# Kernel tuning notes

Hardware: AMD Instinct MI355X
Metric: run time of the kernel (lower is better)

Reference implementation:

```python
import jax, jax.numpy as jnp
import numpy as np

H, MEL, ATT, TXT = 1024, 80, 640, 640   # n_hidden, n_mel, n_attn_channels, n_text+n_speaker
T, TTXT = 600, 128


def setup_inputs() -> dict:
    key = jax.random.key(0)
    ks = jax.random.split(key, 20)
    def w(k, shape, s=0.02):
        return (jax.random.normal(k, shape) * s).astype(jnp.float32)
    return {
        "residual": jax.random.normal(ks[0], (T, 1, MEL), jnp.float32),
        "text": jax.random.normal(ks[1], (TTXT, 1, TXT), jnp.float32),
        # attention_lstm: LSTM(MEL -> H), 1 layer
        "Wih_a": w(ks[2], (4 * H, MEL)), "Whh_a": w(ks[3], (4 * H, H)),
        "bih_a": jnp.zeros(4 * H, jnp.float32), "bhh_a": jnp.zeros(4 * H, jnp.float32),
        # Attention: query/key/value projections + scoring vector v
        "Wq": w(ks[4], (ATT, H)), "Wk": w(ks[5], (ATT, TXT)), "Wv": w(ks[6], (ATT, TXT)),
        "v_w": w(ks[7], (ATT,)),
        # decoder lstm: LSTM(H+ATT -> H), 2 layers
        "Wih0": w(ks[8], (4 * H, H + ATT)), "Whh0": w(ks[9], (4 * H, H)),
        "bih0": jnp.zeros(4 * H, jnp.float32), "bhh0": jnp.zeros(4 * H, jnp.float32),
        "Wih1": w(ks[10], (4 * H, H)), "Whh1": w(ks[11], (4 * H, H)),
        "bih1": jnp.zeros(4 * H, jnp.float32), "bhh1": jnp.zeros(4 * H, jnp.float32),
        # DenseLayer: two tanh(Linear(H,H))
        "D0w": w(ks[12], (H, H)), "D0b": jnp.zeros(H, jnp.float32),
        "D1w": w(ks[13], (H, H)), "D1b": jnp.zeros(H, jnp.float32),
        # Conv1d(H, 2*MEL, kernel=1) == Linear
        "conv_w": w(ks[14], (2 * MEL, H)), "conv_b": jnp.zeros(2 * MEL, jnp.float32),
        # gate layer: Linear(H+ATT, 1)
        "gate_w": w(ks[15], (H + ATT,)), "gate_b": jnp.zeros((), jnp.float32),
    }


def lstm_cell(x, h, c, Wih, Whh, bih, bhh):
    # PyTorch gate order: i, f, g, o
    g = Wih @ x + bih + Whh @ h + bhh
    i, f, gg, o = jnp.split(g, 4)
    c2 = jax.nn.sigmoid(f) * c + jax.nn.sigmoid(i) * jnp.tanh(gg)
    return jax.nn.sigmoid(o) * jnp.tanh(c2), c2


def ar_back_step(residual, text, Wih_a, Whh_a, bih_a, bhh_a, Wq, Wk, Wv, v_w,
                 Wih0, Whh0, bih0, bhh0, Wih1, Whh1, bih1, bhh1,
                 D0w, D0b, D1w, D1b, conv_w, conv_b, gate_w, gate_b):
    res = residual[::-1, 0, :]            # AR_Back_Step flips time; batch=1 squeezed
    txt = text[:, 0, :]                   # [TTXT, TXT]
    K = txt @ Wk.T                        # [TTXT, ATT]  (keys constant over steps)
    V = txt @ Wv.T                        # [TTXT, ATT]
    z = jnp.zeros(H, jnp.float32)
    carry0 = (jnp.zeros(MEL, jnp.float32), z, z, z, z, z, z)

    def step(carry, r_t):
        out_prev, h, c, h0, c0, h1, c1 = carry
        # attention LSTM on previous output
        h, c = lstm_cell(out_prev, h, c, Wih_a, Whh_a, bih_a, bhh_a)
        # additive (Bahdanau-style) attention: v . tanh(q + K)
        q = Wq @ h                                   # [ATT]
        scores = jnp.tanh(q[None, :] + K) @ v_w      # [TTXT]
        attn = jax.nn.softmax(scores)
        ctx = attn @ V                               # [ATT]
        dec_in = jnp.concatenate([h, ctx])           # [H+ATT]
        # 2-layer decoder LSTM
        h0, c0 = lstm_cell(dec_in, h0, c0, Wih0, Whh0, bih0, bhh0)
        h1, c1 = lstm_cell(h0, h1, c1, Wih1, Whh1, bih1, bhh1)
        # DenseLayer (tanh MLP) then 1x1 conv
        d = jnp.tanh(D1w @ jnp.tanh(D0w @ h1 + D0b) + D1b)
        dec_out = conv_w @ d + conv_b                # [2*MEL]
        log_s, b = dec_out[:MEL], dec_out[MEL:]
        out = (r_t - b) / jnp.exp(log_s)             # affine coupling inverse
        gate = jax.nn.sigmoid(gate_w @ dec_in + gate_b)
        return (out, h, c, h0, c0, h1, c1), (out, gate)

    _, (outs, gates) = jax.lax.scan(step, carry0, res)
    total = outs[::-1][:, None, :]                   # flip back, restore batch dim
    return total, gates


def reference(residual, text, Wih_a, Whh_a, bih_a, bhh_a, Wq, Wk, Wv, v_w,
              Wih0, Whh0, bih0, bhh0, Wih1, Whh1, bih1, bhh1,
              D0w, D0b, D1w, D1b, conv_w, conv_b, gate_w, gate_b):
    return ar_back_step(residual, text, Wih_a, Whh_a, bih_a, bhh_a, Wq, Wk, Wv, v_w,
                        Wih0, Whh0, bih0, bhh0, Wih1, Whh1, bih1, bhh1,
                        D0w, D0b, D1w, D1b, conv_w, conv_b, gate_w, gate_b)
```

## Files before the change

### kernel.cpp

```cpp
#include <hip/hip_runtime.h>

#define NBLK 256
#define NTHR 1024

constexpr int H = 1024, MEL = 80, ATT = 640, TXTD = 640, T = 600, TTXT = 128;
constexpr int G4 = 4096, DIN = H + ATT;

constexpr int WS_K     = 0;
constexpr int WS_V     = WS_K + TTXT * ATT;
constexpr int WS_HBUF  = WS_V + TTXT * ATT;
constexpr int WS_H0BUF = WS_HBUF + 2 * H;
constexpr int WS_H1BUF = WS_H0BUF + 2 * H;
constexpr int WS_Q     = WS_H1BUF + 2 * H;
constexpr int WS_W0H   = WS_Q + ATT;
constexpr int WS_U0    = WS_W0H + G4;
constexpr int WS_U1    = WS_U0 + G4;
constexpr int WS_CTX   = WS_U1 + G4;
constexpr int WS_DEN   = WS_CTX + ATT;
constexpr int WS_GH    = WS_DEN + 1;
constexpr int WS_DEC   = (WS_GH + 1 + 15) & ~15;
constexpr int WS_A0    = (WS_DEC + 2 * MEL + 15) & ~15;
constexpr int WS_END   = WS_A0 + H;
constexpr int WS_BAR   = (WS_END + 63) & ~63;

struct Params {
  const float *residual, *text, *Wih_a, *Whh_a, *bih_a, *bhh_a,
      *Wq, *Wk, *Wv, *v_w, *Wih0, *Whh0, *bih0, *bhh0,
      *Wih1, *Whh1, *bih1, *bhh1, *D0w, *D0b, *D1w, *D1b,
      *conv_w, *conv_b, *gate_w, *gate_b;
  float* out;
  float* ws;
};

__device__ __forceinline__ float sigm(float x) { return 1.0f / (1.0f + __expf(-x)); }
__device__ __forceinline__ float ftanh(float x) {
  x = fminf(15.f, fmaxf(-15.f, x));
  float e = __expf(2.f * x);
  return (e - 1.f) / (e + 1.f);
}

__device__ __forceinline__ float aload(const float* p) {
  return __hip_atomic_load(p, __ATOMIC_RELAXED, __HIP_MEMORY_SCOPE_AGENT);
}
__device__ __forceinline__ void astore(float* p, float v) {
  __hip_atomic_store(p, v, __ATOMIC_RELAXED, __HIP_MEMORY_SCOPE_AGENT);
}

__device__ __forceinline__ void gbar(unsigned* bar, unsigned k) {
  asm volatile("s_waitcnt vmcnt(0)" ::: "memory");
  __syncthreads();
  if (threadIdx.x == 0) {
    unsigned* leaf = bar + (blockIdx.x & 15) * 32;
    unsigned o = __hip_atomic_fetch_add(leaf, 1u, __ATOMIC_RELAXED,
                                        __HIP_MEMORY_SCOPE_AGENT);
    if ((o & 15) == 15) {
      unsigned r = __hip_atomic_fetch_add(bar + 512, 1u, __ATOMIC_RELAXED,
                                          __HIP_MEMORY_SCOPE_AGENT);
      if ((r & 15) == 15)
        __hip_atomic_fetch_add(bar + 544, 1u, __ATOMIC_RELAXED,
                               __HIP_MEMORY_SCOPE_AGENT);
    }
    while (__hip_atomic_load(bar + 544, __ATOMIC_RELAXED,
                             __HIP_MEMORY_SCOPE_AGENT) < k)
      __builtin_amdgcn_s_sleep(1);
  }
  __syncthreads();
}

__device__ __forceinline__ float red64(float s) {
#pragma unroll
  for (int off = 32; off; off >>= 1) s += __shfl_xor(s, off, 64);
  return s;
}

__device__ __forceinline__ float dot16pin(float4 w0, float4 w1, float4 w2,
                                          float4 w3, const float* x, int lane) {
  const float4* x4 = (const float4*)x;
  float4 b0 = x4[lane], b1 = x4[lane + 64], b2 = x4[lane + 128],
         b3 = x4[lane + 192];
  float s0 = w0.x * b0.x, s1 = w1.x * b1.x;
  s0 = fmaf(w0.y, b0.y, s0); s1 = fmaf(w1.y, b1.y, s1);
  s0 = fmaf(w0.z, b0.z, s0); s1 = fmaf(w1.z, b1.z, s1);
  s0 = fmaf(w0.w, b0.w, s0); s1 = fmaf(w1.w, b1.w, s1);
  s0 = fmaf(w2.x, b2.x, s0); s1 = fmaf(w3.x, b3.x, s1);
  s0 = fmaf(w2.y, b2.y, s0); s1 = fmaf(w3.y, b3.y, s1);
  s0 = fmaf(w2.z, b2.z, s0); s1 = fmaf(w3.z, b3.z, s1);
  s0 = fmaf(w2.w, b2.w, s0); s1 = fmaf(w3.w, b3.w, s1);
  return s0 + s1;
}

__device__ __forceinline__ float dot16load(const float* __restrict__ w,
                                           const float* __restrict__ x,
                                           int lane) {
  const float4* w4 = (const float4*)w;
  const float4* x4 = (const float4*)x;
  float4 a0 = w4[lane], a1 = w4[lane + 64], a2 = w4[lane + 128],
         a3 = w4[lane + 192];
  float4 b0 = x4[lane], b1 = x4[lane + 64], b2 = x4[lane + 128],
         b3 = x4[lane + 192];
  float s0 = a0.x * b0.x, s1 = a1.x * b1.x;
  s0 = fmaf(a0.y, b0.y, s0); s1 = fmaf(a1.y, b1.y, s1);
  s0 = fmaf(a0.z, b0.z, s0); s1 = fmaf(a1.z, b1.z, s1);
  s0 = fmaf(a0.w, b0.w, s0); s1 = fmaf(a1.w, b1.w, s1);
  s0 = fmaf(a2.x, b2.x, s0); s1 = fmaf(a3.x, b3.x, s1);
  s0 = fmaf(a2.y, b2.y, s0); s1 = fmaf(a3.y, b3.y, s1);
  s0 = fmaf(a2.z, b2.z, s0); s1 = fmaf(a3.z, b3.z, s1);
  s0 = fmaf(a2.w, b2.w, s0); s1 = fmaf(a3.w, b3.w, s1);
  return s0 + s1;
}

__device__ __forceinline__ float wave_dot(const float* __restrict__ w,
                                          const float* __restrict__ x,
                                          int n4, int lane) {
  float s = 0.f;
  const float4* w4 = (const float4*)w;
  const float4* x4 = (const float4*)x;
  for (int i = lane; i < n4; i += 64) {
    float4 a = w4[i];
    float4 b = x4[i];
    s = fmaf(a.x, b.x, s);
    s = fmaf(a.y, b.y, s);
    s = fmaf(a.z, b.z, s);
    s = fmaf(a.w, b.w, s);
  }
  return red64(s);
}

__global__ void __launch_bounds__(NTHR, 4) ar_kernel(Params p) {
  const int b = blockIdx.x;
  const int tid = threadIdx.x;
  const int wave = tid >> 6;
  const int lane = tid & 63;
  const int sg = wave >> 2;
  const int wg = wave & 3;
  const int gw = b * 16 + wave;

  float* ws = p.ws;
  float* Kw = ws + WS_K;
  float* Vw = ws + WS_V;
  float* hbuf = ws + WS_HBUF;
  float* h0buf = ws + WS_H0BUF;
  float* h1buf = ws + WS_H1BUF;
  float* qv = ws + WS_Q;
  float* w0h = ws + WS_W0H;
  float* u0 = ws + WS_U0;
  float* u1 = ws + WS_U1;
  float* ctxa = ws + WS_CTX;
  float* den = ws + WS_DEN;
  float* ghp = ws + WS_GH;
  float* dec = ws + WS_DEC;
  float* a0 = ws + WS_A0;
  unsigned* bar = (unsigned*)(ws + WS_BAR);

  __shared__ __align__(16) float s_h[H];
  __shared__ __align__(16) float s_h0[H];
  __shared__ __align__(16) float s_h1[H];
  __shared__ __align__(16) float s_att[ATT];
  __shared__ __align__(16) float s_out[MEL];
  __shared__ float s_dec[2 * MEL];
  __shared__ float s_red[16];
  __shared__ float s_d[4];
  __shared__ float s_den_sh;

  const int e = 4 * b + sg;
  const int grow = e + wg * H;

  const float4* WA = (const float4*)(p.Whh_a + (size_t)grow * H);
  float4 wa0 = WA[lane], wa1 = WA[lane + 64], wa2 = WA[lane + 128],
         wa3 = WA[lane + 192];
  const float4* W0 = (const float4*)(p.Whh0 + (size_t)gw * H);
  float4 w00 = W0[lane], w01 = W0[lane + 64], w02 = W0[lane + 128],
         w03 = W0[lane + 192];
  const float4* W1 = (const float4*)(p.Whh1 + (size_t)gw * H);
  float4 w10 = W1[lane], w11 = W1[lane + 64], w12 = W1[lane + 128],
         w13 = W1[lane + 192];
  const float4* WI = (const float4*)(p.Wih1 + (size_t)grow * H);
  float4 wi0 = WI[lane], wi1 = WI[lane + 64], wi2 = WI[lane + 128],
         wi3 = WI[lane + 192];
  float4 wma = make_float4(0.f, 0.f, 0.f, 0.f);
  if (lane < MEL / 4)
    wma = ((const float4*)(p.Wih_a + (size_t)grow * MEL))[lane];
  float4 wf = ((const float4*)(p.D0w + (size_t)e * H))[wg * 64 + lane];
  float4 wgd = ((const float4*)(p.D1w + (size_t)e * H))[wg * 64 + lane];
  float4 wcv = make_float4(0.f, 0.f, 0.f, 0.f);
  if (tid < 2 * MEL) wcv = ((const float4*)(p.conv_w + (size_t)tid * H))[b];
  const float ba = p.bih_a[grow] + p.bhh_a[grow];
  const float b0s = p.bih0[grow] + p.bhh0[grow];
  const float b1s = p.bih1[grow] + p.bhh1[grow];

  float c_reg = 0.f, c0_reg = 0.f, c1_reg = 0.f;

  unsigned bk = 0;

  if (b == 0) {
    for (int i = tid; i < 6 * H; i += NTHR) astore(&hbuf[i], 0.f);
  }
  for (int idx = gw; idx < 2 * TTXT * ATT; idx += NBLK * 16) {
    int isV = idx >= TTXT * ATT;
    int rem = isV ? idx - TTXT * ATT : idx;
    int j = rem / ATT;
    int a = rem - j * ATT;
    const float* wrow = (isV ? p.Wv : p.Wk) + a * TXTD;
    float s = wave_dot(wrow, p.text + j * TXTD, TXTD / 4, lane);
    if (lane == 0) astore(&(isV ? Vw : Kw)[j * ATT + a], s);
  }
  gbar(bar, ++bk);

  for (int t = 0; t < T; ++t) {
    const float* h_old = hbuf + (t & 1) * H;
    float* h_new = hbuf + ((t + 1) & 1) * H;
    const float* h0_old = h0buf + (t & 1) * H;
    float* h0_new = h0buf + ((t + 1) & 1) * H;
    const float* h1_old = h1buf + (t & 1) * H;
    float* h1_new = h1buf + ((t + 1) & 1) * H;

    s_h[tid] = aload(h_old + tid);
    s_h0[tid] = aload(h0_old + tid);
    s_h1[tid] = aload(h1_old + tid);
    if (tid < 2 * MEL) s_dec[tid] = aload(dec + tid);
    __syncthreads();
    if (tid < MEL) {
      float o = 0.f;
      if (t != 0) {
        float ls = s_dec[tid] + p.conv_b[tid];
        float bb = s_dec[MEL + tid] + p.conv_b[MEL + tid];
        float r = p.residual[(T - t) * MEL + tid];
        o = (r - bb) * __expf(-ls);
        if (b == 0) p.out[(T - t) * MEL + tid] = o;
      }
      s_out[tid] = o;
    }
    __syncthreads();
    {
      float pa = dot16pin(wa0, wa1, wa2, wa3, s_h, lane);
      if (lane < MEL / 4) {
        float4 bm = ((const float4*)s_out)[lane];
        pa = fmaf(wma.x, bm.x, pa);
        pa = fmaf(wma.y, bm.y, pa);
        pa = fmaf(wma.z, bm.z, pa);
        pa = fmaf(wma.w, bm.w, pa);
      }
      float pu0 = dot16pin(w00, w01, w02, w03, s_h0, lane);
      float pu1 = dot16pin(w10, w11, w12, w13, s_h1, lane);
      pa = red64(pa);
      pu0 = red64(pu0);
      pu1 = red64(pu1);
      if (lane == 0) {
        astore(&u0[gw], pu0);
        astore(&u1[gw], pu1);
        s_red[wave] = pa + ba;
      }
      __syncthreads();
      if (tid < 4) {
        int ee = 4 * b + tid;
        float gi = s_red[tid * 4 + 0], gf = s_red[tid * 4 + 1];
        float gg = s_red[tid * 4 + 2], go = s_red[tid * 4 + 3];
        float c2 = sigm(gf) * c_reg + sigm(gi) * ftanh(gg);
        c_reg = c2;
        astore(&h_new[ee], sigm(go) * ftanh(c2));
      }
    }
    gbar(bar, ++bk);

    s_h[tid] = aload(h_new + tid);
    __syncthreads();
    {
      float s0 = dot16load(p.Wih0 + (size_t)gw * DIN, s_h, lane);
      s0 = red64(s0);
      if (lane == 0) astore(&w0h[gw], s0);
      if (gw < ATT) {
        float q = dot16load(p.Wq + (size_t)gw * H, s_h, lane);
        q = red64(q);
        if (lane == 0) astore(&qv[gw], q);
      } else if (gw == ATT) {
        float q = dot16load(p.gate_w, s_h, lane);
        q = red64(q);
        if (lane == 0) astore(&ghp[0], q);
      }
      if (b == NBLK - 1) {
        for (int i = tid; i < ATT; i += NTHR) astore(&ctxa[i], 0.f);
        if (tid == 0) astore(den, 0.f);
        for (int i = tid; i < 2 * MEL; i += NTHR) astore(&dec[i], 0.f);
      }
    }
    gbar(bar, ++bk);

    if (b < TTXT) {
      if (tid < ATT) s_att[tid] = aload(&qv[tid]);
      __syncthreads();
      const int j = b;
      float sp = 0.f;
      for (int i = tid; i < ATT; i += NTHR)
        sp += ftanh(s_att[i] + Kw[j * ATT + i]) * p.v_w[i];
      sp = red64(sp);
      if (lane == 0) s_red[wave] = sp;
      __syncthreads();
      float sc = 0.f;
#pragma unroll
      for (int k = 0; k < 16; ++k) sc += s_red[k];
      float pj = __expf(sc - 16.f);
      for (int i = tid; i < ATT; i += NTHR)
        atomicAdd(&ctxa[i], pj * Vw[j * ATT + i]);
      if (tid == 0) atomicAdd(den, pj);
    }
    gbar(bar, ++bk);

    {
      if (tid < ATT) s_att[tid] = aload(&ctxa[tid]);
      if (tid == NTHR - 1) s_den_sh = aload(den);
      __syncthreads();
      float wv = 0.f, uu = 0.f;
      if (lane == 0) {
        wv = aload(&w0h[grow]);
        uu = aload(&u0[grow]);
      }
      const float4* W4 = (const float4*)(p.Wih0 + (size_t)grow * DIN + H);
      const float4* X4 = (const float4*)s_att;
      float4 a_ = W4[lane], b_ = X4[lane];
      float4 a2 = W4[lane + 64], b2 = X4[lane + 64];
      float s = a_.x * b_.x;
      s = fmaf(a_.y, b_.y, s); s = fmaf(a_.z, b_.z, s); s = fmaf(a_.w, b_.w, s);
      s = fmaf(a2.x, b2.x, s); s = fmaf(a2.y, b2.y, s);
      s = fmaf(a2.z, b2.z, s); s = fmaf(a2.w, b2.w, s);
      if (lane < 32) {
        float4 a3 = W4[128 + lane], b3 = X4[128 + lane];
        s = fmaf(a3.x, b3.x, s); s = fmaf(a3.y, b3.y, s);
        s = fmaf(a3.z, b3.z, s); s = fmaf(a3.w, b3.w, s);
      }
      s = red64(s);
      float inv = 1.f / s_den_sh;
      if (lane == 0) s_red[wave] = s * inv + wv + uu + b0s;
      if (b == 0 && wave == 15) {
        float gc = wave_dot(p.gate_w + H, s_att, ATT / 4, lane);
        if (lane == 0) {
          float gh = aload(&ghp[0]);
          p.out[T * MEL + t] = sigm(gh + gc * inv + p.gate_b[0]);
        }
      }
      __syncthreads();
      if (tid < 4) {
        int ee = 4 * b + tid;
        float gi = s_red[tid * 4 + 0], gf = s_red[tid * 4 + 1];
        float gg = s_red[tid * 4 + 2], go = s_red[tid * 4 + 3];
        float c2 = sigm(gf) * c0_reg + sigm(gi) * ftanh(gg);
        c0_reg = c2;
        astore(&h0_new[ee], sigm(go) * ftanh(c2));
      }
    }
    gbar(bar, ++bk);

    s_h[tid] = aload(h0_new + tid);
    __syncthreads();
    {
      float u1v = 0.f;
      if (lane == 0) u1v = aload(&u1[grow]);
      float pe = dot16pin(wi0, wi1, wi2, wi3, s_h, lane);
      pe = red64(pe);
      if (lane == 0) s_red[wave] = pe + u1v + b1s;
      __syncthreads();
      if (tid < 4) {
        int ee = 4 * b + tid;
        float gi = s_red[tid * 4 + 0], gf = s_red[tid * 4 + 1];
        float gg = s_red[tid * 4 + 2], go = s_red[tid * 4 + 3];
        float c2 = sigm(gf) * c1_reg + sigm(gi) * ftanh(gg);
        c1_reg = c2;
        astore(&h1_new[ee], sigm(go) * ftanh(c2));
      }
    }
    gbar(bar, ++bk);

    s_h[tid] = aload(h1_new + tid);
    __syncthreads();
    {
      float4 x = ((const float4*)s_h)[wg * 64 + lane];
      float s = wf.x * x.x;
      s = fmaf(wf.y, x.y, s); s = fmaf(wf.z, x.z, s); s = fmaf(wf.w, x.w, s);
      s = red64(s);
      if (lane == 0) s_red[wave] = s;
      __syncthreads();
      if (tid < 4) {
        int r2 = 4 * b + tid;
        float tot = s_red[tid * 4] + s_red[tid * 4 + 1] + s_red[tid * 4 + 2] +
                    s_red[tid * 4 + 3];
        astore(&a0[r2], ftanh(tot + p.D0b[r2]));
      }
    }
    gbar(bar, ++bk);

    s_h[tid] = aload(a0 + tid);
    __syncthreads();
    {
      float4 x = ((const float4*)s_h)[wg * 64 + lane];
      float s = wgd.x * x.x;
      s = fmaf(wgd.y, x.y, s); s = fmaf(wgd.z, x.z, s); s = fmaf(wgd.w, x.w, s);
      s = red64(s);
      if (lane == 0) s_red[wave] = s;
      __syncthreads();
      if (tid < 4) {
        int r2 = 4 * b + tid;
        float tot = s_red[tid * 4] + s_red[tid * 4 + 1] + s_red[tid * 4 + 2] +
                    s_red[tid * 4 + 3];
        s_d[tid] = ftanh(tot + p.D1b[r2]);
      }
      __syncthreads();
      if (tid < 2 * MEL) {
        float acc = wcv.x * s_d[0];
        acc = fmaf(wcv.y, s_d[1], acc);
        acc = fmaf(wcv.z, s_d[2], acc);
        acc = fmaf(wcv.w, s_d[3], acc);
        atomicAdd(&dec[tid], acc);
      }
    }
    gbar(bar, ++bk);
  }

  if (b == 0 && tid < MEL) {
    float ls = aload(&dec[tid]) + p.conv_b[tid];
    float bb = aload(&dec[MEL + tid]) + p.conv_b[MEL + tid];
    float r = p.residual[tid];
    p.out[tid] = (r - bb) * __expf(-ls);
  }
}

extern "C" void kernel_launch(void* const* d_in, const int* in_sizes, int n_in,
                              void* d_out, int out_size, void* d_ws, size_t ws_size,
                              hipStream_t stream) {
  Params hp;
  hp.residual = (const float*)d_in[0];
  hp.text = (const float*)d_in[1];
  hp.Wih_a = (const float*)d_in[2];
  hp.Whh_a = (const float*)d_in[3];
  hp.bih_a = (const float*)d_in[4];
  hp.bhh_a = (const float*)d_in[5];
  hp.Wq = (const float*)d_in[6];
  hp.Wk = (const float*)d_in[7];
  hp.Wv = (const float*)d_in[8];
  hp.v_w = (const float*)d_in[9];
  hp.Wih0 = (const float*)d_in[10];
  hp.Whh0 = (const float*)d_in[11];
  hp.bih0 = (const float*)d_in[12];
  hp.bhh0 = (const float*)d_in[13];
  hp.Wih1 = (const float*)d_in[14];
  hp.Whh1 = (const float*)d_in[15];
  hp.bih1 = (const float*)d_in[16];
  hp.bhh1 = (const float*)d_in[17];
  hp.D0w = (const float*)d_in[18];
  hp.D0b = (const float*)d_in[19];
  hp.D1w = (const float*)d_in[20];
  hp.D1b = (const float*)d_in[21];
  hp.conv_w = (const float*)d_in[22];
  hp.conv_b = (const float*)d_in[23];
  hp.gate_w = (const float*)d_in[24];
  hp.gate_b = (const float*)d_in[25];
  hp.out = (float*)d_out;
  hp.ws = (float*)d_ws;

  hipMemsetAsync((char*)d_ws + (size_t)WS_BAR * sizeof(float), 0, 4096, stream);

  void* args[] = {&hp};
  hipLaunchCooperativeKernel((void*)ar_kernel, dim3(NBLK), dim3(NTHR), args, 0,
                             stream);
}
```

Measured before the change: 27.60 ms.

## Keep per-block weights and partial sums in LDS/registers instead of global workspace

Each wave now computes Whh0/Whh1 partials for its own gate row (grow), so u0, u1 and w0h stay in registers instead of round-tripping through global workspace. The Wih0 rows are staged once into dynamic shared memory, Wq/gate_w rows are pinned in registers, and each block's K/V rows and v_w are cached in LDS for the attention loop. This cuts global loads and atomic-ordered workspace traffic on every timestep. In exchange it uses about 110KB of shared memory per block and more registers, which could limit residency for the cooperative launch.

```diff
diff --git a/kernel.cpp b/kernel.cpp
--- a/kernel.cpp
+++ b/kernel.cpp
@@ -12,16 +12,29 @@
 constexpr int WS_H0BUF = WS_HBUF + 2 * H;
 constexpr int WS_H1BUF = WS_H0BUF + 2 * H;
 constexpr int WS_Q     = WS_H1BUF + 2 * H;
-constexpr int WS_W0H   = WS_Q + ATT;
-constexpr int WS_U0    = WS_W0H + G4;
-constexpr int WS_U1    = WS_U0 + G4;
-constexpr int WS_CTX   = WS_U1 + G4;
+constexpr int WS_CTX   = WS_Q + ATT;
 constexpr int WS_DEN   = WS_CTX + ATT;
 constexpr int WS_GH    = WS_DEN + 1;
 constexpr int WS_DEC   = (WS_GH + 1 + 15) & ~15;
 constexpr int WS_A0    = (WS_DEC + 2 * MEL + 15) & ~15;
 constexpr int WS_END   = WS_A0 + H;
 constexpr int WS_BAR   = (WS_END + 63) & ~63;
+
+constexpr int SM_W0  = 0;
+constexpr int SM_H   = SM_W0 + 16 * DIN;
+constexpr int SM_H0  = SM_H + H;
+constexpr int SM_H1  = SM_H0 + H;
+constexpr int SM_ATT = SM_H1 + H;
+constexpr int SM_K   = SM_ATT + ATT;
+constexpr int SM_V   = SM_K + ATT;
+constexpr int SM_VW  = SM_V + ATT;
+constexpr int SM_OUT = SM_VW + ATT;
+constexpr int SM_DEC = SM_OUT + MEL;
+constexpr int SM_RED = SM_DEC + 2 * MEL;
+constexpr int SM_D   = SM_RED + 16;
+constexpr int SM_DEN = SM_D + 4;
+constexpr int SM_CNT = SM_DEN + 1;
+constexpr size_t SM_BYTES = ((size_t)SM_CNT * 4 + 255) & ~(size_t)255;
 
 struct Params {
   const float *residual, *text, *Wih_a, *Whh_a, *bih_a, *bhh_a,
@@ -89,8 +102,7 @@
   return s0 + s1;
 }
 
-__device__ __forceinline__ float dot16load(const float* __restrict__ w,
-                                           const float* __restrict__ x,
+__device__ __forceinline__ float dot16load(const float* w, const float* x,
                                            int lane) {
   const float4* w4 = (const float4*)w;
   const float4* x4 = (const float4*)x;
@@ -142,9 +154,6 @@
   float* h0buf = ws + WS_H0BUF;
   float* h1buf = ws + WS_H1BUF;
   float* qv = ws + WS_Q;
-  float* w0h = ws + WS_W0H;
-  float* u0 = ws + WS_U0;
-  float* u1 = ws + WS_U1;
   float* ctxa = ws + WS_CTX;
   float* den = ws + WS_DEN;
   float* ghp = ws + WS_GH;
@@ -152,15 +161,20 @@
   float* a0 = ws + WS_A0;
   unsigned* bar = (unsigned*)(ws + WS_BAR);
 
-  __shared__ __align__(16) float s_h[H];
-  __shared__ __align__(16) float s_h0[H];
-  __shared__ __align__(16) float s_h1[H];
-  __shared__ __align__(16) float s_att[ATT];
-  __shared__ __align__(16) float s_out[MEL];
-  __shared__ float s_dec[2 * MEL];
-  __shared__ float s_red[16];
-  __shared__ float s_d[4];
-  __shared__ float s_den_sh;
+  extern __shared__ __align__(16) float smem[];
+  float* s_w0 = smem + SM_W0;
+  float* s_h = smem + SM_H;
+  float* s_h0 = smem + SM_H0;
+  float* s_h1 = smem + SM_H1;
+  float* s_att = smem + SM_ATT;
+  float* s_k = smem + SM_K;
+  float* s_v = smem + SM_V;
+  float* s_vw = smem + SM_VW;
+  float* s_out = smem + SM_OUT;
+  float* s_dec = smem + SM_DEC;
+  float* s_red = smem + SM_RED;
+  float* s_d = smem + SM_D;
+  float* s_den = smem + SM_DEN;
 
   const int e = 4 * b + sg;
   const int grow = e + wg * H;
@@ -168,10 +182,10 @@
   const float4* WA = (const float4*)(p.Whh_a + (size_t)grow * H);
   float4 wa0 = WA[lane], wa1 = WA[lane + 64], wa2 = WA[lane + 128],
          wa3 = WA[lane + 192];
-  const float4* W0 = (const float4*)(p.Whh0 + (size_t)gw * H);
+  const float4* W0 = (const float4*)(p.Whh0 + (size_t)grow * H);
   float4 w00 = W0[lane], w01 = W0[lane + 64], w02 = W0[lane + 128],
          w03 = W0[lane + 192];
-  const float4* W1 = (const float4*)(p.Whh1 + (size_t)gw * H);
+  const float4* W1 = (const float4*)(p.Whh1 + (size_t)grow * H);
   float4 w10 = W1[lane], w11 = W1[lane + 64], w12 = W1[lane + 128],
          w13 = W1[lane + 192];
   const float4* WI = (const float4*)(p.Wih1 + (size_t)grow * H);
@@ -184,11 +198,27 @@
   float4 wgd = ((const float4*)(p.D1w + (size_t)e * H))[wg * 64 + lane];
   float4 wcv = make_float4(0.f, 0.f, 0.f, 0.f);
   if (tid < 2 * MEL) wcv = ((const float4*)(p.conv_w + (size_t)tid * H))[b];
+  const float* xsrc = nullptr;
+  if (gw < ATT) xsrc = p.Wq + (size_t)gw * H;
+  else if (gw == ATT) xsrc = p.gate_w;
+  float4 wx0 = make_float4(0.f, 0.f, 0.f, 0.f), wx1 = wx0, wx2 = wx0, wx3 = wx0;
+  if (xsrc) {
+    const float4* X = (const float4*)xsrc;
+    wx0 = X[lane]; wx1 = X[lane + 64]; wx2 = X[lane + 128]; wx3 = X[lane + 192];
+  }
   const float ba = p.bih_a[grow] + p.bhh_a[grow];
   const float b0s = p.bih0[grow] + p.bhh0[grow];
   const float b1s = p.bih1[grow] + p.bhh1[grow];
 
+  {
+    const float4* src = (const float4*)(p.Wih0 + (size_t)grow * DIN);
+    float4* dst = (float4*)(s_w0 + wave * DIN);
+    for (int i = lane; i < DIN / 4; i += 64) dst[i] = src[i];
+  }
+  for (int i = tid; i < ATT; i += NTHR) s_vw[i] = p.v_w[i];
+
   float c_reg = 0.f, c0_reg = 0.f, c1_reg = 0.f;
+  float u0_reg = 0.f, u1_reg = 0.f, w0h_reg = 0.f;
 
   unsigned bk = 0;
 
@@ -205,6 +235,12 @@
     if (lane == 0) astore(&(isV ? Vw : Kw)[j * ATT + a], s);
   }
   gbar(bar, ++bk);
+  if (b < TTXT) {
+    for (int i = tid; i < ATT; i += NTHR) {
+      s_k[i] = aload(&Kw[b * ATT + i]);
+      s_v[i] = aload(&Vw[b * ATT + i]);
+    }
+  }
 
   for (int t = 0; t < T; ++t) {
     const float* h_old = hbuf + (t & 1) * H;
@@ -243,13 +279,9 @@
       float pu0 = dot16pin(w00, w01, w02, w03, s_h0, lane);
       float pu1 = dot16pin(w10, w11, w12, w13, s_h1, lane);
       pa = red64(pa);
-      pu0 = red64(pu0);
-      pu1 = red64(pu1);
-      if (lane == 0) {
-        astore(&u0[gw], pu0);
-        astore(&u1[gw], pu1);
-        s_red[wave] = pa + ba;
-      }
+      u0_reg = red64(pu0);
+      u1_reg = red64(pu1);
+      if (lane == 0) s_red[wave] = pa + ba;
       __syncthreads();
       if (tid < 4) {
         int ee = 4 * b + tid;
@@ -265,17 +297,15 @@
     s_h[tid] = aload(h_new + tid);
     __syncthreads();
     {
-      float s0 = dot16load(p.Wih0 + (size_t)gw * DIN, s_h, lane);
-      s0 = red64(s0);
-      if (lane == 0) astore(&w0h[gw], s0);
-      if (gw < ATT) {
-        float q = dot16load(p.Wq + (size_t)gw * H, s_h, lane);
+      float s0 = dot16load(s_w0 + wave * DIN, s_h, lane);
+      w0h_reg = red64(s0);
+      if (xsrc) {
+        float q = dot16pin(wx0, wx1, wx2, wx3, s_h, lane);
         q = red64(q);
-        if (lane == 0) astore(&qv[gw], q);
-      } else if (gw == ATT) {
-        float q = dot16load(p.gate_w, s_h, lane);
-        q = red64(q);
-        if (lane == 0) astore(&ghp[0], q);
+        if (lane == 0) {
+          if (gw < ATT) astore(&qv[gw], q);
+          else astore(&ghp[0], q);
+        }
       }
       if (b == NBLK - 1) {
         for (int i = tid; i < ATT; i += NTHR) astore(&ctxa[i], 0.f);
@@ -288,10 +318,9 @@
     if (b < TTXT) {
       if (tid < ATT) s_att[tid] = aload(&qv[tid]);
       __syncthreads();
-      const int j = b;
       float sp = 0.f;
       for (int i = tid; i < ATT; i += NTHR)
-        sp += ftanh(s_att[i] + Kw[j * ATT + i]) * p.v_w[i];
+        sp += ftanh(s_att[i] + s_k[i]) * s_vw[i];
       sp = red64(sp);
       if (lane == 0) s_red[wave] = sp;
       __syncthreads();
@@ -300,21 +329,16 @@
       for (int k = 0; k < 16; ++k) sc += s_red[k];
       float pj = __expf(sc - 16.f);
       for (int i = tid; i < ATT; i += NTHR)
-        atomicAdd(&ctxa[i], pj * Vw[j * ATT + i]);
+        atomicAdd(&ctxa[i], pj * s_v[i]);
       if (tid == 0) atomicAdd(den, pj);
     }
     gbar(bar, ++bk);
 
     {
       if (tid < ATT) s_att[tid] = aload(&ctxa[tid]);
-      if (tid == NTHR - 1) s_den_sh = aload(den);
-      __syncthreads();
-      float wv = 0.f, uu = 0.f;
-      if (lane == 0) {
-        wv = aload(&w0h[grow]);
-        uu = aload(&u0[grow]);
-      }
-      const float4* W4 = (const float4*)(p.Wih0 + (size_t)grow * DIN + H);
+      if (tid == NTHR - 1) s_den[0] = aload(den);
+      __syncthreads();
+      const float4* W4 = (const float4*)(s_w0 + wave * DIN + H);
       const float4* X4 = (const float4*)s_att;
       float4 a_ = W4[lane], b_ = X4[lane];
       float4 a2 = W4[lane + 64], b2 = X4[lane + 64];
@@ -328,8 +352,8 @@
         s = fmaf(a3.z, b3.z, s); s = fmaf(a3.w, b3.w, s);
       }
       s = red64(s);
-      float inv = 1.f / s_den_sh;
-      if (lane == 0) s_red[wave] = s * inv + wv + uu + b0s;
+      float inv = 1.f / s_den[0];
+      if (lane == 0) s_red[wave] = s * inv + w0h_reg + u0_reg + b0s;
       if (b == 0 && wave == 15) {
         float gc = wave_dot(p.gate_w + H, s_att, ATT / 4, lane);
         if (lane == 0) {
@@ -352,11 +376,9 @@
     s_h[tid] = aload(h0_new + tid);
     __syncthreads();
     {
-      float u1v = 0.f;
-      if (lane == 0) u1v = aload(&u1[grow]);
       float pe = dot16pin(wi0, wi1, wi2, wi3, s_h, lane);
       pe = red64(pe);
-      if (lane == 0) s_red[wave] = pe + u1v + b1s;
+      if (lane == 0) s_red[wave] = pe + u1_reg + b1s;
       __syncthreads();
       if (tid < 4) {
         int ee = 4 * b + tid;
@@ -458,6 +480,6 @@
   hipMemsetAsync((char*)d_ws + (size_t)WS_BAR * sizeof(float), 0, 4096, stream);
 
   void* args[] = {&hp};
-  hipLaunchCooperativeKernel((void*)ar_kernel, dim3(NBLK), dim3(NTHR), args, 0,
-                             stream);
-}
+  hipLaunchCooperativeKernel((void*)ar_kernel, dim3(NBLK), dim3(NTHR), args,
+                             (uint32_t)SM_BYTES, stream);
+}
```

Result: faster. 26.28 ms (-4.8%).
